# Performance work log

Measured on AMD Instinct MI355X. Metric: run time of the kernel, lower is better.

The kernel has to match this reference:

```python
import jax, jax.numpy as jnp
import numpy as np

NX = 65536   # spatial cells
T = 32       # time points
H = 128      # MLP hidden width
DX = 1.0     # spatial resolution (init kwarg dx)
S0, S1 = -1.0, 1.0  # fixed stencil (learn_stencil=False)


def setup_inputs() -> dict:
    key = jax.random.key(0)
    k1, k2, k3, k4 = jax.random.split(key, 4)
    t = jnp.arange(T, dtype=jnp.float32) * 0.01          # time grid, dt=0.01
    u0 = jax.random.uniform(k1, (NX,), jnp.float32)      # initial state
    inv_sqrt_h = jnp.float32(1.0 / np.sqrt(H))
    W1 = jax.random.normal(k2, (1, H), jnp.float32)
    W2 = jax.random.normal(k3, (H, H), jnp.float32) * inv_sqrt_h
    W3 = jax.random.normal(k4, (H, 1), jnp.float32) * inv_sqrt_h
    D = jnp.full((1,), 0.01, jnp.float32)                # diffusion coefficient
    BC = jnp.zeros((2, 1), jnp.float32)                  # Dirichlet BC values
    return {"t": t, "u0": u0, "W1": W1, "W2": W2, "W3": W3, "D": D, "BC": BC}


def _flux(u, W1, W2, W3, D, BC):
    # per-cell MLP (func_nn): Linear->Tanh->Linear->Tanh->Linear, no bias, no sigmoid
    h = jnp.tanh(u[:, None] @ W1)        # [Nx, H]
    h = jnp.tanh(h @ W2)                 # [Nx, H]
    a = (h @ W3)[:, 0]                   # [Nx]
    a_plus = jax.nn.relu(a)
    a_min = -jax.nn.relu(-a)
    d = D[0]
    # left fluxes
    lb = d * (S0 * u[0] + S1 * BC[0, 0]) - a_plus[0] / DX * (-S0 * u[0] - S1 * BC[0, 0])
    ln = d * (S0 * u[1:] + S1 * u[:-1]) - a_plus[1:] / DX * (-S0 * u[1:] - S1 * u[:-1])
    left = jnp.concatenate([lb[None], ln])
    # right fluxes
    rb = d * (S0 * u[-1] + S1 * BC[1, 0]) - a_min[-1] / DX * (S0 * u[-1] + S1 * BC[1, 0])
    rn = d * (S0 * u[:-1] + S1 * u[1:]) - a_min[:-1] / DX * (S0 * u[:-1] + S1 * u[1:])
    right = jnp.concatenate([rn, rb[None]])
    return left + right


def reference(t, u0, W1, W2, W3, D, BC):
    # Neural-ODE integration of du/dt = flux_kernel(u); fixed-step RK4 over grid t
    f = lambda u: _flux(u, W1, W2, W3, D, BC)

    def step(u, dt):
        k1 = f(u)
        k2 = f(u + 0.5 * dt * k1)
        k3 = f(u + 0.5 * dt * k2)
        k4 = f(u + dt * k3)
        un = u + (dt / 6.0) * (k1 + 2.0 * k2 + 2.0 * k3 + k4)
        return un, un

    _, us = jax.lax.scan(step, u0, jnp.diff(t))
    return jnp.concatenate([u0[None], us], axis=0)  # [T, Nx]
```

## Files before the change

### kernel.cpp

```cpp
#include <hip/hip_runtime.h>

#define NXC 65536
#define TT 32
#define HH 128
#define TABNP 65
#define TABLO (-0.25f)
#define TABINV 32.0f
#define OUTW 64
#define VC 5
#define WINW 320
#define HALO 128

typedef unsigned short u16;

__device__ __forceinline__ float bf2f(u16 b) {
    union { unsigned int u; float f; } v; v.u = ((unsigned int)b) << 16; return v.f;
}
__device__ __forceinline__ u16 f2bf(float f) {
    union { float f; unsigned int u; } v; v.f = f;
    return (u16)((v.u + 0x7fffu + ((v.u >> 16) & 1u)) >> 16);
}
__device__ __forceinline__ bool is_bf16_mode(const void* t) {
    return ((const u16*)t)[1] != 0;
}

#if __has_builtin(__builtin_amdgcn_exp2f)
#define EXP2F(x) __builtin_amdgcn_exp2f(x)
#else
#define EXP2F(x) exp2f(x)
#endif
#if __has_builtin(__builtin_amdgcn_rcpf)
#define RCPF(x) __builtin_amdgcn_rcpf(x)
#else
#define RCPF(x) (1.0f / (x))
#endif

__device__ __forceinline__ float fast_tanh(float x) {
    float e = EXP2F(x * 2.8853900817779268f);
    return 1.0f - 2.0f * RCPF(e + 1.0f);
}

__device__ __forceinline__ float bperm(int byte_addr, float v) {
    return __int_as_float(
        __builtin_amdgcn_ds_bpermute(byte_addr, __float_as_int(v)));
}

__global__ __launch_bounds__(256) void tabbuild_kernel(
    const void* traw, const void* W1, const void* W2, const void* W3,
    float* __restrict__ atab) {
    __shared__ float h1s[4][HH];
    bool bf = is_bf16_mode(traw);
    int tid = threadIdx.x;
    int lane = tid & 63;
    int w = tid >> 6;
    int e = blockIdx.x * 4 + w;
    float uin = TABLO + (float)e * (1.0f / TABINV);

#pragma unroll
    for (int h = 0; h < 2; ++h) {
        int k = lane + h * 64;
        float w1k = bf ? bf2f(((const u16*)W1)[k]) : ((const float*)W1)[k];
        h1s[w][k] = fast_tanh(uin * w1k);
    }
    float acc0 = 0.f, acc1 = 0.f;
    if (bf) {
        for (int k = 0; k < HH; ++k) {
            float h1k = h1s[w][k];
            acc0 = fmaf(h1k, bf2f(((const u16*)W2)[k * HH + lane]), acc0);
            acc1 = fmaf(h1k, bf2f(((const u16*)W2)[k * HH + lane + 64]), acc1);
        }
    } else {
        for (int k = 0; k < HH; ++k) {
            float h1k = h1s[w][k];
            acc0 = fmaf(h1k, ((const float*)W2)[k * HH + lane], acc0);
            acc1 = fmaf(h1k, ((const float*)W2)[k * HH + lane + 64], acc1);
        }
    }
    float t0 = fast_tanh(acc0);
    float t1 = fast_tanh(acc1);
    float w3a = bf ? bf2f(((const u16*)W3)[lane]) : ((const float*)W3)[lane];
    float w3b = bf ? bf2f(((const u16*)W3)[lane + 64]) : ((const float*)W3)[lane + 64];
    float p = t0 * w3a + t1 * w3b;
#pragma unroll
    for (int sh = 1; sh < 64; sh <<= 1) p += __shfl_xor(p, sh, 64);
    if (lane == 0 && e < TABNP) atab[e] = p;
}

__global__ __launch_bounds__(256) void fused_kernel(
    const void* traw, const void* u0raw, const void* Draw, const void* BCraw,
    const float* __restrict__ atab, void* outbase) {
    __shared__ float t32s[TT];

    int tid = threadIdx.x;
    bool bf = is_bf16_mode(traw);
    if (tid < TT)
        t32s[tid] = bf ? bf2f(((const u16*)traw)[tid]) : ((const float*)traw)[tid];

    float d   = bf ? bf2f(((const u16*)Draw)[0])  : ((const float*)Draw)[0];
    float bc0 = bf ? bf2f(((const u16*)BCraw)[0]) : ((const float*)BCraw)[0];
    float bc1 = bf ? bf2f(((const u16*)BCraw)[1]) : ((const float*)BCraw)[1];

    int lane = tid & 63;
    float tabv = atab[lane];
    float tabs = atab[lane + 1] - tabv;

    int wid = blockIdx.x * 4 + (tid >> 6);
    int gb = wid * OUTW - HALO + lane * VC;
    int i0 = lane * VC;

    float v[VC], ub[VC], kacc[VC], dpa[VC], dma[VC];
    bool gok[VC], isl[VC], isr[VC], own[VC];
#pragma unroll
    for (int j = 0; j < VC; ++j) {
        int g = gb + j;
        int i = i0 + j;
        gok[j] = (g >= 0) && (g < NXC);
        isl[j] = (g == 0);
        isr[j] = (g == NXC - 1);
        own[j] = (i >= HALO) && (i < HALO + OUTW);
        float x = 0.f;
        if (gok[j])
            x = bf ? bf2f(((const u16*)u0raw)[g]) : ((const float*)u0raw)[g];
        v[j] = x;
        ub[j] = x;
        if (own[j]) {
            if (bf) ((u16*)outbase)[g] = ((const u16*)u0raw)[g];
            else    ((float*)outbase)[g] = x;
        }
    }
    __syncthreads();

    for (int step = 0; step < TT - 1; ++step) {
        float dt = t32s[step + 1] - t32s[step];
        float dt2 = 0.5f * dt, dt6 = dt * (1.0f / 6.0f);

#pragma unroll
        for (int j = 0; j < VC; ++j) {
            float f = fmaf(v[j], TABINV, (-TABLO) * TABINV);
            f = fminf(fmaxf(f, 0.0f), 62.999f);
            int e0 = (int)f;
            float frac = f - (float)e0;
            int ad = e0 << 2;
            float a = fmaf(frac, bperm(ad, tabs), bperm(ad, tabv));
            dpa[j] = d + fmaxf(a, 0.f);
            dma[j] = d - fminf(a, 0.f);
            kacc[j] = 0.f;
        }
#pragma unroll
        for (int s = 0; s < 4; ++s) {
            int sigma = step * 4 + s;
            float cnext = (s < 2) ? dt2 : dt;
            float wgt = (s == 1 || s == 2) ? 2.f : 1.f;
            float vup = __shfl_up(v[VC - 1], 1, 64);
            float vdn = __shfl_down(v[0], 1, 64);
#pragma unroll
            for (int j = 0; j < VC; ++j) {
                float vc = v[j];
                float vl = (j == 0) ? vup : v[j - 1];
                float vr = (j == VC - 1) ? vdn : v[j + 1];
                vl = isl[j] ? bc0 : vl;
                vr = isr[j] ? bc1 : vr;
                float kv = (vl - vc) * dpa[j] + (vr - vc) * dma[j];
                kacc[j] = fmaf(wgt, kv, kacc[j]);
                int i = i0 + j;
                bool act = gok[j] && (i > sigma) && (i < WINW - 1 - sigma);
                float vn = (s < 3) ? fmaf(cnext, kv, ub[j])
                                   : fmaf(dt6, kacc[j], ub[j]);
                if (act) {
                    v[j] = vn;
                    if (s == 3) ub[j] = vn;
                }
            }
        }
        size_t rb = (size_t)(step + 1) * NXC;
#pragma unroll
        for (int j = 0; j < VC; ++j) {
            if (own[j]) {
                if (bf) ((u16*)outbase)[rb + gb + j] = f2bf(ub[j]);
                else    ((float*)outbase)[rb + gb + j] = ub[j];
            }
        }
    }
}

extern "C" void kernel_launch(void* const* d_in, const int* in_sizes, int n_in,
                              void* d_out, int out_size, void* d_ws,
                              size_t ws_size, hipStream_t stream) {
    const void* t  = d_in[0];
    const void* u0 = d_in[1];
    const void* W1 = d_in[2];
    const void* W2 = d_in[3];
    const void* W3 = d_in[4];
    const void* Dp = d_in[5];
    const void* BC = d_in[6];

    float* atab = (float*)d_ws;

    tabbuild_kernel<<<17, 256, 0, stream>>>(t, W1, W2, W3, atab);
    fused_kernel<<<NXC / (OUTW * 4), 256, 0, stream>>>(t, u0, Dp, BC, atab, d_out);
}
```

Baseline: 114.3 us.

## Exchange a 4-cell halo once per RK4 step and specialize boundary wavefronts

Each lane now gathers a 13-cell extended window (its own 5 cells plus 4 neighbours on each side) through shuffles once per time step. All four RK4 stages are then computed from registers, with no per-stage cross-lane shuffles, by shrinking the valid range by one cell each stage. The cost is redundant recomputation of halo cells and more table lookups, since 11 cells per lane are evaluated instead of 5. A templated fast path drops the boundary and activity checks for interior wavefronts, and only the edge wavefronts keep the guarded path.

Result: slower. 133.2 us (+16.6%).

```diff
diff --git a/kernel.cpp b/kernel.cpp
--- a/kernel.cpp
+++ b/kernel.cpp
@@ -86,6 +86,53 @@
     if (lane == 0 && e < TABNP) atab[e] = p;
 }
 
+template <bool SLOW>
+__device__ __forceinline__ void do_stages(
+    float (&e0)[13], float (&ec)[13], const float (&dpa)[13],
+    const float (&dma)[13], float (&kacc)[VC], float (&v)[VC],
+    float dt2, float dt, float dt6, int step, int lane, int gE,
+    float bc0, float bc1) {
+    float kv[13];
+#pragma unroll
+    for (int s = 0; s < 4; ++s) {
+        float cnext = (s < 2) ? dt2 : dt;
+        float wgt = (s == 1 || s == 2) ? 2.f : 1.f;
+        int sigma = step * 4 + s;
+#pragma unroll
+        for (int m = 1; m <= 11; ++m) {
+            if (m < 1 + s || m > 11 - s) continue;
+            float vc = ec[m], vl = ec[m - 1], vr = ec[m + 1];
+            if (SLOW) {
+                int g = gE + m;
+                vl = (g == 0) ? bc0 : vl;
+                vr = (g == NXC - 1) ? bc1 : vr;
+            }
+            kv[m] = (vl - vc) * dpa[m] + (vr - vc) * dma[m];
+        }
+#pragma unroll
+        for (int m = 1; m <= 11; ++m) {
+            if (m < 1 + s || m > 11 - s) continue;
+            bool isown = (m >= 4 && m <= 8);
+            if (isown) kacc[m - 4] = fmaf(wgt, kv[m], kacc[m - 4]);
+            float vn = (s < 3) ? fmaf(cnext, kv[m], e0[m])
+                               : fmaf(dt6, kacc[m - 4], e0[m]);
+            if (SLOW) {
+                int g = gE + m;
+                int i = lane * VC + m - 4;
+                bool act = (g >= 0) && (g < NXC) && (i > sigma) &&
+                           (i < WINW - 1 - sigma);
+                if (act) {
+                    ec[m] = vn;
+                    if (s == 3) v[m - 4] = vn;
+                }
+            } else {
+                ec[m] = vn;
+                if (s == 3) v[m - 4] = vn;
+            }
+        }
+    }
+}
+
 __global__ __launch_bounds__(256) void fused_kernel(
     const void* traw, const void* u0raw, const void* Draw, const void* BCraw,
     const float* __restrict__ atab, void* outbase) {
@@ -105,24 +152,20 @@
     float tabs = atab[lane + 1] - tabv;
 
     int wid = blockIdx.x * 4 + (tid >> 6);
-    int gb = wid * OUTW - HALO + lane * VC;
-    int i0 = lane * VC;
-
-    float v[VC], ub[VC], kacc[VC], dpa[VC], dma[VC];
-    bool gok[VC], isl[VC], isr[VC], own[VC];
+    bool slow = (wid < 2) || (wid >= 1022);
+    int gE = wid * OUTW - HALO + lane * VC - 4;
+
+    float v[VC];
+    bool own[VC];
 #pragma unroll
     for (int j = 0; j < VC; ++j) {
-        int g = gb + j;
-        int i = i0 + j;
-        gok[j] = (g >= 0) && (g < NXC);
-        isl[j] = (g == 0);
-        isr[j] = (g == NXC - 1);
+        int g = gE + 4 + j;
+        int i = lane * VC + j;
         own[j] = (i >= HALO) && (i < HALO + OUTW);
+        bool ok = (g >= 0) && (g < NXC);
         float x = 0.f;
-        if (gok[j])
-            x = bf ? bf2f(((const u16*)u0raw)[g]) : ((const float*)u0raw)[g];
+        if (ok) x = bf ? bf2f(((const u16*)u0raw)[g]) : ((const float*)u0raw)[g];
         v[j] = x;
-        ub[j] = x;
         if (own[j]) {
             if (bf) ((u16*)outbase)[g] = ((const u16*)u0raw)[g];
             else    ((float*)outbase)[g] = x;
@@ -134,50 +177,46 @@
         float dt = t32s[step + 1] - t32s[step];
         float dt2 = 0.5f * dt, dt6 = dt * (1.0f / 6.0f);
 
-#pragma unroll
-        for (int j = 0; j < VC; ++j) {
-            float f = fmaf(v[j], TABINV, (-TABLO) * TABINV);
+        float e0[13], ec[13];
+        e0[4] = v[0]; e0[5] = v[1]; e0[6] = v[2]; e0[7] = v[3]; e0[8] = v[4];
+        e0[0] = __shfl_up(v[1], 1, 64);
+        e0[1] = __shfl_up(v[2], 1, 64);
+        e0[2] = __shfl_up(v[3], 1, 64);
+        e0[3] = __shfl_up(v[4], 1, 64);
+        e0[9]  = __shfl_down(v[0], 1, 64);
+        e0[10] = __shfl_down(v[1], 1, 64);
+        e0[11] = __shfl_down(v[2], 1, 64);
+        e0[12] = __shfl_down(v[3], 1, 64);
+
+        float dpa[13], dma[13];
+#pragma unroll
+        for (int m = 1; m <= 11; ++m) {
+            float f = fmaf(e0[m], TABINV, 8.0f);
             f = fminf(fmaxf(f, 0.0f), 62.999f);
-            int e0 = (int)f;
-            float frac = f - (float)e0;
-            int ad = e0 << 2;
+            int eidx = (int)f;
+            float frac = f - (float)eidx;
+            int ad = eidx << 2;
             float a = fmaf(frac, bperm(ad, tabs), bperm(ad, tabv));
-            dpa[j] = d + fmaxf(a, 0.f);
-            dma[j] = d - fminf(a, 0.f);
-            kacc[j] = 0.f;
-        }
-#pragma unroll
-        for (int s = 0; s < 4; ++s) {
-            int sigma = step * 4 + s;
-            float cnext = (s < 2) ? dt2 : dt;
-            float wgt = (s == 1 || s == 2) ? 2.f : 1.f;
-            float vup = __shfl_up(v[VC - 1], 1, 64);
-            float vdn = __shfl_down(v[0], 1, 64);
-#pragma unroll
-            for (int j = 0; j < VC; ++j) {
-                float vc = v[j];
-                float vl = (j == 0) ? vup : v[j - 1];
-                float vr = (j == VC - 1) ? vdn : v[j + 1];
-                vl = isl[j] ? bc0 : vl;
-                vr = isr[j] ? bc1 : vr;
-                float kv = (vl - vc) * dpa[j] + (vr - vc) * dma[j];
-                kacc[j] = fmaf(wgt, kv, kacc[j]);
-                int i = i0 + j;
-                bool act = gok[j] && (i > sigma) && (i < WINW - 1 - sigma);
-                float vn = (s < 3) ? fmaf(cnext, kv, ub[j])
-                                   : fmaf(dt6, kacc[j], ub[j]);
-                if (act) {
-                    v[j] = vn;
-                    if (s == 3) ub[j] = vn;
-                }
-            }
-        }
+            dpa[m] = d + fmaxf(a, 0.f);
+            dma[m] = d - fminf(a, 0.f);
+        }
+#pragma unroll
+        for (int m = 0; m < 13; ++m) ec[m] = e0[m];
+        float kacc[VC] = {0.f, 0.f, 0.f, 0.f, 0.f};
+
+        if (!slow)
+            do_stages<false>(e0, ec, dpa, dma, kacc, v, dt2, dt, dt6, step,
+                             lane, gE, bc0, bc1);
+        else
+            do_stages<true>(e0, ec, dpa, dma, kacc, v, dt2, dt, dt6, step,
+                            lane, gE, bc0, bc1);
+
         size_t rb = (size_t)(step + 1) * NXC;
 #pragma unroll
         for (int j = 0; j < VC; ++j) {
             if (own[j]) {
-                if (bf) ((u16*)outbase)[rb + gb + j] = f2bf(ub[j]);
-                else    ((float*)outbase)[rb + gb + j] = ub[j];
+                if (bf) ((u16*)outbase)[rb + gE + 4 + j] = f2bf(v[j]);
+                else    ((float*)outbase)[rb + gE + 4 + j] = v[j];
             }
         }
     }
```

## Halve per-wave output width and specialize interior waves without boundary predicates

Applied to the files above, without the earlier changes.

Each wave now produces 32 output cells instead of 64, with a larger halo, so twice as many blocks are launched. The grid is split into three launches: two boundary launches that keep the boundary-condition and active-cell checks, and one interior launch that drops all those predicates. The time-step constants are precomputed once in an extra table-build block instead of being derived in every block. The aim is more resident waves to hide the latency of the serial RK4 stencil chain, at the cost of roughly twice as much redundant halo compute, extra launch overhead, and some out-of-range u0 reads at the edges of the interior launch.

Result: slower. 183.5 us (+60.6%).

```diff
diff --git a/kernel.cpp b/kernel.cpp
--- a/kernel.cpp
+++ b/kernel.cpp
@@ -6,10 +6,10 @@
 #define TABNP 65
 #define TABLO (-0.25f)
 #define TABINV 32.0f
-#define OUTW 64
+#define OUTW 32
 #define VC 5
 #define WINW 320
-#define HALO 128
+#define HALO 144
 
 typedef unsigned short u16;
 
@@ -47,7 +47,7 @@
 
 __global__ __launch_bounds__(256) void tabbuild_kernel(
     const void* traw, const void* W1, const void* W2, const void* W3,
-    float* __restrict__ atab) {
+    float* __restrict__ atab, float2* __restrict__ dtab) {
     __shared__ float h1s[4][HH];
     bool bf = is_bf16_mode(traw);
     int tid = threadIdx.x;
@@ -56,6 +56,18 @@
     int e = blockIdx.x * 4 + w;
     float uin = TABLO + (float)e * (1.0f / TABINV);
 
+    if (blockIdx.x == 17) {
+        if (w == 0 && lane < TT - 1) {
+            float t0 = bf ? bf2f(((const u16*)traw)[lane])
+                          : ((const float*)traw)[lane];
+            float t1 = bf ? bf2f(((const u16*)traw)[lane + 1])
+                          : ((const float*)traw)[lane + 1];
+            float dt = t1 - t0;
+            dtab[lane] = make_float2(0.5f * dt, dt * (1.0f / 6.0f));
+        }
+        return;
+    }
+
 #pragma unroll
     for (int h = 0; h < 2; ++h) {
         int k = lane + h * 64;
@@ -86,15 +98,16 @@
     if (lane == 0 && e < TABNP) atab[e] = p;
 }
 
+template <bool SLOW>
 __global__ __launch_bounds__(256) void fused_kernel(
     const void* traw, const void* u0raw, const void* Draw, const void* BCraw,
-    const float* __restrict__ atab, void* outbase) {
-    __shared__ float t32s[TT];
+    const float* __restrict__ atab, const float2* __restrict__ dtab,
+    void* outbase, int widbase) {
+    __shared__ float2 dts[TT - 1];
 
     int tid = threadIdx.x;
     bool bf = is_bf16_mode(traw);
-    if (tid < TT)
-        t32s[tid] = bf ? bf2f(((const u16*)traw)[tid]) : ((const float*)traw)[tid];
+    if (tid < TT - 1) dts[tid] = dtab[tid];
 
     float d   = bf ? bf2f(((const u16*)Draw)[0])  : ((const float*)Draw)[0];
     float bc0 = bf ? bf2f(((const u16*)BCraw)[0]) : ((const float*)BCraw)[0];
@@ -104,7 +117,7 @@
     float tabv = atab[lane];
     float tabs = atab[lane + 1] - tabv;
 
-    int wid = blockIdx.x * 4 + (tid >> 6);
+    int wid = widbase + blockIdx.x * 4 + (tid >> 6);
     int gb = wid * OUTW - HALO + lane * VC;
     int i0 = lane * VC;
 
@@ -114,9 +127,9 @@
     for (int j = 0; j < VC; ++j) {
         int g = gb + j;
         int i = i0 + j;
-        gok[j] = (g >= 0) && (g < NXC);
-        isl[j] = (g == 0);
-        isr[j] = (g == NXC - 1);
+        gok[j] = SLOW ? ((g >= 0) && (g < NXC)) : true;
+        isl[j] = SLOW && (g == 0);
+        isr[j] = SLOW && (g == NXC - 1);
         own[j] = (i >= HALO) && (i < HALO + OUTW);
         float x = 0.f;
         if (gok[j])
@@ -131,12 +144,13 @@
     __syncthreads();
 
     for (int step = 0; step < TT - 1; ++step) {
-        float dt = t32s[step + 1] - t32s[step];
-        float dt2 = 0.5f * dt, dt6 = dt * (1.0f / 6.0f);
+        float2 dd = dts[step];
+        float dt2 = dd.x, dt6 = dd.y;
+        float dt = dt2 + dt2;
 
 #pragma unroll
         for (int j = 0; j < VC; ++j) {
-            float f = fmaf(v[j], TABINV, (-TABLO) * TABINV);
+            float f = fmaf(v[j], TABINV, 8.0f);
             f = fminf(fmaxf(f, 0.0f), 62.999f);
             int e0 = (int)f;
             float frac = f - (float)e0;
@@ -148,7 +162,6 @@
         }
 #pragma unroll
         for (int s = 0; s < 4; ++s) {
-            int sigma = step * 4 + s;
             float cnext = (s < 2) ? dt2 : dt;
             float wgt = (s == 1 || s == 2) ? 2.f : 1.f;
             float vup = __shfl_up(v[VC - 1], 1, 64);
@@ -158,15 +171,23 @@
                 float vc = v[j];
                 float vl = (j == 0) ? vup : v[j - 1];
                 float vr = (j == VC - 1) ? vdn : v[j + 1];
-                vl = isl[j] ? bc0 : vl;
-                vr = isr[j] ? bc1 : vr;
+                if (SLOW) {
+                    vl = isl[j] ? bc0 : vl;
+                    vr = isr[j] ? bc1 : vr;
+                }
                 float kv = (vl - vc) * dpa[j] + (vr - vc) * dma[j];
                 kacc[j] = fmaf(wgt, kv, kacc[j]);
-                int i = i0 + j;
-                bool act = gok[j] && (i > sigma) && (i < WINW - 1 - sigma);
                 float vn = (s < 3) ? fmaf(cnext, kv, ub[j])
                                    : fmaf(dt6, kacc[j], ub[j]);
-                if (act) {
+                if (SLOW) {
+                    int sigma = step * 4 + s;
+                    int i = i0 + j;
+                    bool act = gok[j] && (i > sigma) && (i < WINW - 1 - sigma);
+                    if (act) {
+                        v[j] = vn;
+                        if (s == 3) ub[j] = vn;
+                    }
+                } else {
                     v[j] = vn;
                     if (s == 3) ub[j] = vn;
                 }
@@ -195,7 +216,14 @@
     const void* BC = d_in[6];
 
     float* atab = (float*)d_ws;
-
-    tabbuild_kernel<<<17, 256, 0, stream>>>(t, W1, W2, W3, atab);
-    fused_kernel<<<NXC / (OUTW * 4), 256, 0, stream>>>(t, u0, Dp, BC, atab, d_out);
-}
+    float2* dtab = (float2*)(atab + 66);
+
+    tabbuild_kernel<<<18, 256, 0, stream>>>(t, W1, W2, W3, atab, dtab);
+
+    fused_kernel<true><<<1, 256, 0, stream>>>(t, u0, Dp, BC, atab, dtab,
+                                              d_out, 0);
+    fused_kernel<false><<<510, 256, 0, stream>>>(t, u0, Dp, BC, atab, dtab,
+                                                 d_out, 4);
+    fused_kernel<true><<<1, 256, 0, stream>>>(t, u0, Dp, BC, atab, dtab,
+                                              d_out, 2044);
+}
```
